# Kernel tuning notes

Hardware: AMD Instinct MI355X
Metric: run time of the kernel (lower is better)

Reference implementation:

```python
import jax, jax.numpy as jnp
import numpy as np

N = 8192  # number of nodes
F = 8     # feature dim


def setup_inputs() -> dict:
    key = jax.random.key(0)
    ks = jax.random.split(key, 24)
    inp = {
        "adj": jax.random.uniform(ks[0], (N, N), jnp.float32),
        "dist_from_prev": jax.random.uniform(ks[1], (N,), jnp.float32),
        "dist_to_start": jax.random.uniform(ks[2], (N,), jnp.float32),
    }
    dims = {"l0": (2, F), "l1": (F, F), "pol": (F, 1), "val": (F, 1)}
    i = 3
    for name, (din, dout) in dims.items():
        inp[f"W1_{name}"] = jax.random.normal(ks[i], (din, dout), jnp.float32) * 0.3; i += 1
        inp[f"b1_{name}"] = jax.random.normal(ks[i], (dout,), jnp.float32) * 0.1; i += 1
        inp[f"W2_{name}"] = jax.random.normal(ks[i], (dout, dout), jnp.float32) * 0.3; i += 1
        inp[f"b2_{name}"] = jax.random.normal(ks[i], (dout,), jnp.float32) * 0.1; i += 1
    return inp


def _mlp(x, adj, W1, b1, W2, b2):
    # GIN-style layer: aggregate then 2-layer MLP
    h = adj @ x                     # [N, din] aggregation (memory bound)
    h = jax.nn.relu(h @ W1 + b1)    # [N, dout]
    return h @ W2 + b2              # [N, dout]


def reference(adj, dist_from_prev, dist_to_start,
              W1_l0, b1_l0, W2_l0, b2_l0,
              W1_l1, b1_l1, W2_l1, b2_l1,
              W1_pol, b1_pol, W2_pol, b2_pol,
              W1_val, b1_val, W2_val, b2_val):
    cur = jnp.stack([dist_from_prev, dist_to_start], axis=1)  # [N, 2]
    # hidden GIN layers + relu (dropout is identity in eval mode)
    cur = jax.nn.relu(_mlp(cur, adj, W1_l0, b1_l0, W2_l0, b2_l0))
    cur = jax.nn.relu(_mlp(cur, adj, W1_l1, b1_l1, W2_l1, b2_l1))
    policy = jax.nn.softmax(_mlp(cur, adj, W1_pol, b1_pol, W2_pol, b2_pol)[:, 0], axis=0)  # [N]
    value = _mlp(cur, adj, W1_val, b1_val, W2_val, b2_val)[:, 0]  # [N]
    m = value.mean()
    std = jnp.sqrt(jnp.mean((value - m) ** 2) + 1e-10)
    normalized_value = (value - m) / std
    return policy, normalized_value
```

## Files before the change

### kernel.cpp

```cpp
#include <hip/hip_runtime.h>
#include <hip/hip_bf16.h>
#include <math.h>

#define NN 8192
typedef unsigned int u32;
typedef unsigned char u8;

__device__ __forceinline__ u32 bf16_rtne(float f) {
  u32 u = __float_as_uint(f);
  return (u + 0x7fffu + ((u >> 16) & 1u)) >> 16;
}
__device__ __forceinline__ float bf_lo(u32 d) { return __uint_as_float(d << 16); }
__device__ __forceinline__ float bf_hi(u32 d) { return __uint_as_float(d & 0xffff0000u); }

__global__ __launch_bounds__(256) void pass1_kernel(
    const float* __restrict__ adj, u8* __restrict__ adj8,
    const float* __restrict__ dfp, const float* __restrict__ dts,
    const float* __restrict__ W1, const float* __restrict__ b1,
    const float* __restrict__ W2, const float* __restrict__ b2,
    float* __restrict__ cur) {
  const int wave = threadIdx.x >> 6, lane = threadIdx.x & 63;
  const int row0 = blockIdx.x * 16 + wave * 4;
  float acc0[4] = {0.f, 0.f, 0.f, 0.f};
  float acc1[4] = {0.f, 0.f, 0.f, 0.f};

  float4 A[4], Xp, Xs;
  {
    const int k = 4 * lane;
    Xp = *(const float4*)(dfp + k);
    Xs = *(const float4*)(dts + k);
#pragma unroll
    for (int r = 0; r < 4; ++r)
      A[r] = *(const float4*)(adj + (size_t)(row0 + r) * NN + k);
  }
  for (int k0 = 0; k0 < NN; k0 += 256) {
    float4 B[4], Yp, Ys;
    if (k0 + 256 < NN) {
      const int k = k0 + 256 + 4 * lane;
      Yp = *(const float4*)(dfp + k);
      Ys = *(const float4*)(dts + k);
#pragma unroll
      for (int r = 0; r < 4; ++r)
        B[r] = *(const float4*)(adj + (size_t)(row0 + r) * NN + k);
    } else {
      Yp = Xp; Ys = Xs;
#pragma unroll
      for (int r = 0; r < 4; ++r) B[r] = A[r];
    }
    const float pv[4] = {Xp.x, Xp.y, Xp.z, Xp.w};
    const float sv[4] = {Xs.x, Xs.y, Xs.z, Xs.w};
#pragma unroll
    for (int r = 0; r < 4; ++r) {
      const float av[4] = {A[r].x, A[r].y, A[r].z, A[r].w};
#pragma unroll
      for (int c = 0; c < 4; ++c) {
        acc0[r] = fmaf(av[c], pv[c], acc0[r]);
        acc1[r] = fmaf(av[c], sv[c], acc1[r]);
      }
      u32 q0 = (u32)fmaf(av[0], 255.f, 0.5f);
      u32 q1 = (u32)fmaf(av[1], 255.f, 0.5f);
      u32 q2 = (u32)fmaf(av[2], 255.f, 0.5f);
      u32 q3 = (u32)fmaf(av[3], 255.f, 0.5f);
      ((u32*)(adj8 + (size_t)(row0 + r) * NN + k0))[lane] =
          q0 | (q1 << 8) | (q2 << 16) | (q3 << 24);
    }
#pragma unroll
    for (int r = 0; r < 4; ++r) A[r] = B[r];
    Xp = Yp; Xs = Ys;
  }
#pragma unroll
  for (int r = 0; r < 4; ++r) {
    for (int off = 32; off; off >>= 1) {
      acc0[r] += __shfl_xor(acc0[r], off, 64);
      acc1[r] += __shfl_xor(acc1[r], off, 64);
    }
  }
  const int j = lane & 7;
#pragma unroll
  for (int r = 0; r < 4; ++r) {
    float z = fmaf(acc0[r], W1[0 * 8 + j], fmaf(acc1[r], W1[1 * 8 + j], b1[j]));
    z = fmaxf(z, 0.f);
    float o = b2[j];
#pragma unroll
    for (int jj = 0; jj < 8; ++jj)
      o = fmaf(__shfl(z, jj, 64), W2[jj * 8 + j], o);
    if (lane < 8) cur[(size_t)(row0 + r) * 8 + j] = fmaxf(o, 0.f);
  }
}

template <int HEADS>
__global__ __launch_bounds__(512) void pass23_kernel(
    const u8* __restrict__ adj8, const float* __restrict__ x,
    const float* __restrict__ W1, const float* __restrict__ b1,
    const float* __restrict__ W2, const float* __restrict__ b2,
    const float* __restrict__ W1v, const float* __restrict__ b1v,
    const float* __restrict__ W2v, const float* __restrict__ b2v,
    float* __restrict__ out0, float* __restrict__ out1) {
  __shared__ u32 xT[8][NN / 2];
  const int tid = threadIdx.x;
  const int wave = tid >> 6, lane = tid & 63;
  const int row0 = blockIdx.x * 32 + wave * 4;

  uint4 A[4];
#pragma unroll
  for (int r = 0; r < 4; ++r)
    A[r] = *(const uint4*)(adj8 + (size_t)(row0 + r) * NN + 16 * lane);

  const float inv255 = 1.f / 255.f;
  for (int p = tid; p < NN / 2; p += 512) {
    const float* r0 = x + (size_t)p * 16;
    float4 a0 = *(const float4*)(r0);
    float4 b0 = *(const float4*)(r0 + 4);
    float4 a1 = *(const float4*)(r0 + 8);
    float4 c1 = *(const float4*)(r0 + 12);
    const float e0[8] = {a0.x, a0.y, a0.z, a0.w, b0.x, b0.y, b0.z, b0.w};
    const float e1[8] = {a1.x, a1.y, a1.z, a1.w, c1.x, c1.y, c1.z, c1.w};
#pragma unroll
    for (int jj = 0; jj < 8; ++jj)
      xT[jj][p] = bf16_rtne(e0[jj] * inv255) | (bf16_rtne(e1[jj] * inv255) << 16);
  }
  __syncthreads();

  float acc[4][8] = {};
  for (int k0 = 0; k0 < NN; k0 += 1024) {
    uint4 B[4];
    if (k0 + 1024 < NN) {
#pragma unroll
      for (int r = 0; r < 4; ++r)
        B[r] = *(const uint4*)(adj8 + (size_t)(row0 + r) * NN + (k0 + 1024) +
                               16 * lane);
    } else {
#pragma unroll
      for (int r = 0; r < 4; ++r) B[r] = A[r];
    }
    float av[4][16];
#pragma unroll
    for (int r = 0; r < 4; ++r) {
      const u32 dw[4] = {A[r].x, A[r].y, A[r].z, A[r].w};
#pragma unroll
      for (int t = 0; t < 16; ++t)
        av[r][t] = (float)((dw[t >> 2] >> (8 * (t & 3))) & 0xffu);
    }
    const u32* xrow;
#pragma unroll
    for (int jj = 0; jj < 8; ++jj) {
      xrow = &xT[jj][0];
      uint4 xp0 = *((const uint4*)xrow + (k0 >> 3) + 2 * lane);
      uint4 xp1 = *((const uint4*)xrow + (k0 >> 3) + 2 * lane + 1);
      float xf[16];
      xf[0] = bf_lo(xp0.x);  xf[1] = bf_hi(xp0.x);
      xf[2] = bf_lo(xp0.y);  xf[3] = bf_hi(xp0.y);
      xf[4] = bf_lo(xp0.z);  xf[5] = bf_hi(xp0.z);
      xf[6] = bf_lo(xp0.w);  xf[7] = bf_hi(xp0.w);
      xf[8] = bf_lo(xp1.x);  xf[9] = bf_hi(xp1.x);
      xf[10] = bf_lo(xp1.y); xf[11] = bf_hi(xp1.y);
      xf[12] = bf_lo(xp1.z); xf[13] = bf_hi(xp1.z);
      xf[14] = bf_lo(xp1.w); xf[15] = bf_hi(xp1.w);
#pragma unroll
      for (int r = 0; r < 4; ++r)
#pragma unroll
        for (int t = 0; t < 16; ++t)
          acc[r][jj] = fmaf(av[r][t], xf[t], acc[r][jj]);
    }
#pragma unroll
    for (int r = 0; r < 4; ++r) A[r] = B[r];
  }
#pragma unroll
  for (int r = 0; r < 4; ++r)
#pragma unroll
    for (int jj = 0; jj < 8; ++jj)
      for (int off = 32; off; off >>= 1)
        acc[r][jj] += __shfl_xor(acc[r][jj], off, 64);

  if (HEADS == 0) {
    const int j = lane & 7;
#pragma unroll
    for (int r = 0; r < 4; ++r) {
      float z = b1[j];
#pragma unroll
      for (int d = 0; d < 8; ++d) z = fmaf(acc[r][d], W1[d * 8 + j], z);
      z = fmaxf(z, 0.f);
      float o = b2[j];
#pragma unroll
      for (int jj = 0; jj < 8; ++jj)
        o = fmaf(__shfl(z, jj, 64), W2[jj * 8 + j], o);
      if (lane < 8) out0[(size_t)(row0 + r) * 8 + j] = fmaxf(o, 0.f);
    }
  } else {
    if (lane == 0) {
#pragma unroll
      for (int r = 0; r < 4; ++r) {
        float zp = b1[0], zv = b1v[0];
#pragma unroll
        for (int d = 0; d < 8; ++d) {
          zp = fmaf(acc[r][d], W1[d], zp);
          zv = fmaf(acc[r][d], W1v[d], zv);
        }
        zp = fmaxf(zp, 0.f);
        zv = fmaxf(zv, 0.f);
        out0[row0 + r] = fmaf(zp, W2[0], b2[0]);
        out1[row0 + r] = fmaf(zv, W2v[0], b2v[0]);
      }
    }
  }
}

__global__ __launch_bounds__(1024) void reduce_finalize_kernel(
    float* __restrict__ out) {
  const int tid = threadIdx.x, wave = tid >> 6, lane = tid & 63;
  __shared__ float sa[16], sb[16], sc[4];

  float4 l0 = *(const float4*)(out + tid * 8);
  float4 l1 = *(const float4*)(out + tid * 8 + 4);
  float4 v0 = *(const float4*)(out + NN + tid * 8);
  float4 v1 = *(const float4*)(out + NN + tid * 8 + 4);
  const float lv[8] = {l0.x, l0.y, l0.z, l0.w, l1.x, l1.y, l1.z, l1.w};
  const float vv[8] = {v0.x, v0.y, v0.z, v0.w, v1.x, v1.y, v1.z, v1.w};

  float m = -3.4e38f, s = 0.f;
#pragma unroll
  for (int i = 0; i < 8; ++i) {
    m = fmaxf(m, lv[i]);
    s += vv[i];
  }
  for (int off = 32; off; off >>= 1) {
    m = fmaxf(m, __shfl_xor(m, off, 64));
    s += __shfl_xor(s, off, 64);
  }
  if (lane == 0) { sa[wave] = m; sb[wave] = s; }
  __syncthreads();
  if (tid == 0) {
    float mm = sa[0], ss = sb[0];
    for (int i = 1; i < 16; ++i) { mm = fmaxf(mm, sa[i]); ss += sb[i]; }
    sc[0] = mm; sc[1] = ss * (1.f / NN);
  }
  __syncthreads();
  m = sc[0];
  const float mean = sc[1];

  float el[8];
  float e = 0.f, v2 = 0.f;
#pragma unroll
  for (int i = 0; i < 8; ++i) {
    el[i] = expf(lv[i] - m);
    e += el[i];
    float d = vv[i] - mean;
    v2 = fmaf(d, d, v2);
  }
  for (int off = 32; off; off >>= 1) {
    e += __shfl_xor(e, off, 64);
    v2 += __shfl_xor(v2, off, 64);
  }
  if (lane == 0) { sa[wave] = e; sb[wave] = v2; }
  __syncthreads();
  if (tid == 0) {
    float ee = sa[0], vvv = sb[0];
    for (int i = 1; i < 16; ++i) { ee += sa[i]; vvv += sb[i]; }
    sc[2] = 1.f / ee;
    sc[3] = 1.f / sqrtf(vvv * (1.f / NN) + 1e-10f);
  }
  __syncthreads();
  const float inv_e = sc[2], inv_std = sc[3];
  float4 o0, o1, w0, w1;
  o0.x = el[0] * inv_e; o0.y = el[1] * inv_e;
  o0.z = el[2] * inv_e; o0.w = el[3] * inv_e;
  o1.x = el[4] * inv_e; o1.y = el[5] * inv_e;
  o1.z = el[6] * inv_e; o1.w = el[7] * inv_e;
  w0.x = (vv[0] - mean) * inv_std; w0.y = (vv[1] - mean) * inv_std;
  w0.z = (vv[2] - mean) * inv_std; w0.w = (vv[3] - mean) * inv_std;
  w1.x = (vv[4] - mean) * inv_std; w1.y = (vv[5] - mean) * inv_std;
  w1.z = (vv[6] - mean) * inv_std; w1.w = (vv[7] - mean) * inv_std;
  *(float4*)(out + tid * 8) = o0;
  *(float4*)(out + tid * 8 + 4) = o1;
  *(float4*)(out + NN + tid * 8) = w0;
  *(float4*)(out + NN + tid * 8 + 4) = w1;
}

extern "C" void kernel_launch(void* const* d_in, const int* in_sizes, int n_in,
                              void* d_out, int out_size, void* d_ws,
                              size_t ws_size, hipStream_t stream) {
  const float* adj = (const float*)d_in[0];
  const float* dfp = (const float*)d_in[1];
  const float* dts = (const float*)d_in[2];
  const float* W1_l0 = (const float*)d_in[3];
  const float* b1_l0 = (const float*)d_in[4];
  const float* W2_l0 = (const float*)d_in[5];
  const float* b2_l0 = (const float*)d_in[6];
  const float* W1_l1 = (const float*)d_in[7];
  const float* b1_l1 = (const float*)d_in[8];
  const float* W2_l1 = (const float*)d_in[9];
  const float* b2_l1 = (const float*)d_in[10];
  const float* W1_pol = (const float*)d_in[11];
  const float* b1_pol = (const float*)d_in[12];
  const float* W2_pol = (const float*)d_in[13];
  const float* b2_pol = (const float*)d_in[14];
  const float* W1_val = (const float*)d_in[15];
  const float* b1_val = (const float*)d_in[16];
  const float* W2_val = (const float*)d_in[17];
  const float* b2_val = (const float*)d_in[18];

  u8* adj8 = (u8*)d_ws;
  float* curA = (float*)((char*)d_ws + (size_t)NN * NN);
  float* curB = curA + NN * 8;
  float* logits = (float*)d_out;
  float* value = logits + NN;

  pass1_kernel<<<NN / 16, 256, 0, stream>>>(adj, adj8, dfp, dts, W1_l0, b1_l0,
                                            W2_l0, b2_l0, curA);
  pass23_kernel<0><<<NN / 32, 512, 0, stream>>>(
      adj8, curA, W1_l1, b1_l1, W2_l1, b2_l1, W1_l1, b1_l1, W2_l1, b2_l1,
      curB, curB);
  pass23_kernel<1><<<NN / 32, 512, 0, stream>>>(
      adj8, curB, W1_pol, b1_pol, W2_pol, b2_pol, W1_val, b1_val, W2_val,
      b2_val, logits, value);
  reduce_finalize_kernel<<<1, 1024, 0, stream>>>((float*)d_out);
}
```

Baseline: 152.4 us.

## Quantize features to uint8 per-column and use integer dot4 for aggregation

The bf16 feature staging and the float FMAs on dequantized adjacency bytes are replaced by per-column uint8 quantization of the features. The scale comes from a global max gathered through per-block partial maxima written by the previous kernel. The aggregation then runs as packed 8-bit integer dot products (udot4) with u32 accumulators, which greatly cuts ALU work per adjacency byte, and is rescaled to float at the end. In exchange, the features lose precision (8 bits instead of bf16), and there is extra work for a transpose in shared memory and for the cross-block max reduction.

```diff
diff --git a/kernel.cpp b/kernel.cpp
--- a/kernel.cpp
+++ b/kernel.cpp
@@ -1,26 +1,31 @@
 #include <hip/hip_runtime.h>
-#include <hip/hip_bf16.h>
 #include <math.h>
 
 #define NN 8192
 typedef unsigned int u32;
 typedef unsigned char u8;
 
-__device__ __forceinline__ u32 bf16_rtne(float f) {
-  u32 u = __float_as_uint(f);
-  return (u + 0x7fffu + ((u >> 16) & 1u)) >> 16;
-}
-__device__ __forceinline__ float bf_lo(u32 d) { return __uint_as_float(d << 16); }
-__device__ __forceinline__ float bf_hi(u32 d) { return __uint_as_float(d & 0xffff0000u); }
+__device__ __forceinline__ u32 dot4(u32 a, u32 b, u32 c) {
+#if __has_builtin(__builtin_amdgcn_udot4)
+  return __builtin_amdgcn_udot4(a, b, c, false);
+#else
+  c += (a & 0xffu) * (b & 0xffu);
+  c += ((a >> 8) & 0xffu) * ((b >> 8) & 0xffu);
+  c += ((a >> 16) & 0xffu) * ((b >> 16) & 0xffu);
+  c += (a >> 24) * (b >> 24);
+  return c;
+#endif
+}
 
 __global__ __launch_bounds__(256) void pass1_kernel(
     const float* __restrict__ adj, u8* __restrict__ adj8,
     const float* __restrict__ dfp, const float* __restrict__ dts,
     const float* __restrict__ W1, const float* __restrict__ b1,
     const float* __restrict__ W2, const float* __restrict__ b2,
-    float* __restrict__ cur) {
+    float* __restrict__ cur, float* __restrict__ partial) {
   const int wave = threadIdx.x >> 6, lane = threadIdx.x & 63;
   const int row0 = blockIdx.x * 16 + wave * 4;
+  __shared__ float w1red[4][8];
   float acc0[4] = {0.f, 0.f, 0.f, 0.f};
   float acc1[4] = {0.f, 0.f, 0.f, 0.f};
 
@@ -76,6 +81,7 @@
     }
   }
   const int j = lane & 7;
+  float mx = 0.f;
 #pragma unroll
   for (int r = 0; r < 4; ++r) {
     float z = fmaf(acc0[r], W1[0 * 8 + j], fmaf(acc1[r], W1[1 * 8 + j], b1[j]));
@@ -84,19 +90,33 @@
 #pragma unroll
     for (int jj = 0; jj < 8; ++jj)
       o = fmaf(__shfl(z, jj, 64), W2[jj * 8 + j], o);
-    if (lane < 8) cur[(size_t)(row0 + r) * 8 + j] = fmaxf(o, 0.f);
+    float val = fmaxf(o, 0.f);
+    if (lane < 8) cur[(size_t)(row0 + r) * 8 + j] = val;
+    mx = fmaxf(mx, val);
+  }
+  if (lane < 8) w1red[wave][lane] = mx;
+  __syncthreads();
+  if (wave == 0 && lane < 8) {
+    float m2 = fmaxf(fmaxf(w1red[0][lane], w1red[1][lane]),
+                     fmaxf(w1red[2][lane], w1red[3][lane]));
+    partial[blockIdx.x * 8 + lane] = m2;
   }
 }
 
 template <int HEADS>
 __global__ __launch_bounds__(512) void pass23_kernel(
     const u8* __restrict__ adj8, const float* __restrict__ x,
+    const float* __restrict__ partial, int nprod,
     const float* __restrict__ W1, const float* __restrict__ b1,
     const float* __restrict__ W2, const float* __restrict__ b2,
     const float* __restrict__ W1v, const float* __restrict__ b1v,
     const float* __restrict__ W2v, const float* __restrict__ b2v,
-    float* __restrict__ out0, float* __restrict__ out1) {
-  __shared__ u32 xT[8][NN / 2];
+    float* __restrict__ out0, float* __restrict__ out1,
+    float* __restrict__ partial_out) {
+  __shared__ u32 sxR[NN * 2];
+  __shared__ u32 sxT[8 * 2048];
+  __shared__ float swred[8][8];
+  __shared__ float sqs[8], sds[8];
   const int tid = threadIdx.x;
   const int wave = tid >> 6, lane = tid & 63;
   const int row0 = blockIdx.x * 32 + wave * 4;
@@ -106,22 +126,64 @@
   for (int r = 0; r < 4; ++r)
     A[r] = *(const uint4*)(adj8 + (size_t)(row0 + r) * NN + 16 * lane);
 
-  const float inv255 = 1.f / 255.f;
-  for (int p = tid; p < NN / 2; p += 512) {
-    const float* r0 = x + (size_t)p * 16;
-    float4 a0 = *(const float4*)(r0);
-    float4 b0 = *(const float4*)(r0 + 4);
-    float4 a1 = *(const float4*)(r0 + 8);
-    float4 c1 = *(const float4*)(r0 + 12);
-    const float e0[8] = {a0.x, a0.y, a0.z, a0.w, b0.x, b0.y, b0.z, b0.w};
-    const float e1[8] = {a1.x, a1.y, a1.z, a1.w, c1.x, c1.y, c1.z, c1.w};
-#pragma unroll
-    for (int jj = 0; jj < 8; ++jj)
-      xT[jj][p] = bf16_rtne(e0[jj] * inv255) | (bf16_rtne(e1[jj] * inv255) << 16);
-  }
-  __syncthreads();
-
-  float acc[4][8] = {};
+  float pm[8] = {0.f, 0.f, 0.f, 0.f, 0.f, 0.f, 0.f, 0.f};
+  if (tid < nprod) {
+    float4 a = *(const float4*)(partial + tid * 8);
+    float4 b = *(const float4*)(partial + tid * 8 + 4);
+    pm[0] = a.x; pm[1] = a.y; pm[2] = a.z; pm[3] = a.w;
+    pm[4] = b.x; pm[5] = b.y; pm[6] = b.z; pm[7] = b.w;
+  }
+  for (int off = 32; off; off >>= 1)
+#pragma unroll
+    for (int j = 0; j < 8; ++j) pm[j] = fmaxf(pm[j], __shfl_xor(pm[j], off, 64));
+  if (lane == 0)
+#pragma unroll
+    for (int j = 0; j < 8; ++j) swred[wave][j] = pm[j];
+  __syncthreads();
+  if (tid < 8) {
+    float m2 = 0.f;
+#pragma unroll
+    for (int w = 0; w < 8; ++w) m2 = fmaxf(m2, swred[w][tid]);
+    m2 = fmaxf(m2, 1e-20f);
+    sqs[tid] = 255.f / m2;
+    sds[tid] = m2 / 65025.f;
+  }
+  __syncthreads();
+
+  float qs[8];
+#pragma unroll
+  for (int j = 0; j < 8; ++j) qs[j] = sqs[j];
+  for (int base = 0; base < NN; base += 512) {
+    const int row = base + tid;
+    float4 a = *(const float4*)(x + (size_t)row * 8);
+    float4 b = *(const float4*)(x + (size_t)row * 8 + 4);
+    u32 q0 = (u32)fmaf(a.x, qs[0], 0.5f), q1 = (u32)fmaf(a.y, qs[1], 0.5f);
+    u32 q2 = (u32)fmaf(a.z, qs[2], 0.5f), q3 = (u32)fmaf(a.w, qs[3], 0.5f);
+    u32 q4 = (u32)fmaf(b.x, qs[4], 0.5f), q5 = (u32)fmaf(b.y, qs[5], 0.5f);
+    u32 q6 = (u32)fmaf(b.z, qs[6], 0.5f), q7 = (u32)fmaf(b.w, qs[7], 0.5f);
+    uint2 pk;
+    pk.x = q0 | (q1 << 8) | (q2 << 16) | (q3 << 24);
+    pk.y = q4 | (q5 << 8) | (q6 << 16) | (q7 << 24);
+    ((uint2*)sxR)[row] = pk;
+  }
+  __syncthreads();
+
+  {
+    const int jj = tid & 7, g = tid >> 3;
+    const int dw = jj >> 2, sh = 8 * (jj & 3);
+#pragma unroll
+    for (int i = 0; i < 32; ++i) {
+      const int p = g + 64 * i;
+      u32 w = 0;
+#pragma unroll
+      for (int m = 0; m < 4; ++m)
+        w |= (((sxR[(4 * p + m) * 2 + dw] >> sh) & 0xffu) << (8 * m));
+      sxT[jj * 2048 + p] = w;
+    }
+  }
+  __syncthreads();
+
+  u32 acc[4][8] = {};
   for (int k0 = 0; k0 < NN; k0 += 1024) {
     uint4 B[4];
     if (k0 + 1024 < NN) {
@@ -133,34 +195,21 @@
 #pragma unroll
       for (int r = 0; r < 4; ++r) B[r] = A[r];
     }
-    float av[4][16];
+    uint4 xq[8];
+#pragma unroll
+    for (int jj = 0; jj < 8; ++jj)
+      xq[jj] = ((const uint4*)sxT)[jj * 512 + (k0 >> 4) + lane];
 #pragma unroll
     for (int r = 0; r < 4; ++r) {
-      const u32 dw[4] = {A[r].x, A[r].y, A[r].z, A[r].w};
-#pragma unroll
-      for (int t = 0; t < 16; ++t)
-        av[r][t] = (float)((dw[t >> 2] >> (8 * (t & 3))) & 0xffu);
-    }
-    const u32* xrow;
-#pragma unroll
-    for (int jj = 0; jj < 8; ++jj) {
-      xrow = &xT[jj][0];
-      uint4 xp0 = *((const uint4*)xrow + (k0 >> 3) + 2 * lane);
-      uint4 xp1 = *((const uint4*)xrow + (k0 >> 3) + 2 * lane + 1);
-      float xf[16];
-      xf[0] = bf_lo(xp0.x);  xf[1] = bf_hi(xp0.x);
-      xf[2] = bf_lo(xp0.y);  xf[3] = bf_hi(xp0.y);
-      xf[4] = bf_lo(xp0.z);  xf[5] = bf_hi(xp0.z);
-      xf[6] = bf_lo(xp0.w);  xf[7] = bf_hi(xp0.w);
-      xf[8] = bf_lo(xp1.x);  xf[9] = bf_hi(xp1.x);
-      xf[10] = bf_lo(xp1.y); xf[11] = bf_hi(xp1.y);
-      xf[12] = bf_lo(xp1.z); xf[13] = bf_hi(xp1.z);
-      xf[14] = bf_lo(xp1.w); xf[15] = bf_hi(xp1.w);
-#pragma unroll
-      for (int r = 0; r < 4; ++r)
-#pragma unroll
-        for (int t = 0; t < 16; ++t)
-          acc[r][jj] = fmaf(av[r][t], xf[t], acc[r][jj]);
+#pragma unroll
+      for (int jj = 0; jj < 8; ++jj) {
+        u32 c = acc[r][jj];
+        c = dot4(A[r].x, xq[jj].x, c);
+        c = dot4(A[r].y, xq[jj].y, c);
+        c = dot4(A[r].z, xq[jj].z, c);
+        c = dot4(A[r].w, xq[jj].w, c);
+        acc[r][jj] = c;
+      }
     }
 #pragma unroll
     for (int r = 0; r < 4; ++r) A[r] = B[r];
@@ -170,21 +219,40 @@
 #pragma unroll
     for (int jj = 0; jj < 8; ++jj)
       for (int off = 32; off; off >>= 1)
-        acc[r][jj] += __shfl_xor(acc[r][jj], off, 64);
+        acc[r][jj] += (u32)__shfl_xor((int)acc[r][jj], off, 64);
+  float dsc[8];
+#pragma unroll
+  for (int j = 0; j < 8; ++j) dsc[j] = sds[j];
+  float h[4][8];
+#pragma unroll
+  for (int r = 0; r < 4; ++r)
+#pragma unroll
+    for (int jj = 0; jj < 8; ++jj) h[r][jj] = (float)acc[r][jj] * dsc[jj];
 
   if (HEADS == 0) {
     const int j = lane & 7;
+    float mxv = 0.f;
 #pragma unroll
     for (int r = 0; r < 4; ++r) {
       float z = b1[j];
 #pragma unroll
-      for (int d = 0; d < 8; ++d) z = fmaf(acc[r][d], W1[d * 8 + j], z);
+      for (int d = 0; d < 8; ++d) z = fmaf(h[r][d], W1[d * 8 + j], z);
       z = fmaxf(z, 0.f);
       float o = b2[j];
 #pragma unroll
       for (int jj = 0; jj < 8; ++jj)
         o = fmaf(__shfl(z, jj, 64), W2[jj * 8 + j], o);
-      if (lane < 8) out0[(size_t)(row0 + r) * 8 + j] = fmaxf(o, 0.f);
+      float val = fmaxf(o, 0.f);
+      if (lane < 8) out0[(size_t)(row0 + r) * 8 + j] = val;
+      mxv = fmaxf(mxv, val);
+    }
+    if (lane < 8) swred[wave][lane] = mxv;
+    __syncthreads();
+    if (wave == 0 && lane < 8) {
+      float m2 = 0.f;
+#pragma unroll
+      for (int w = 0; w < 8; ++w) m2 = fmaxf(m2, swred[w][lane]);
+      partial_out[blockIdx.x * 8 + lane] = m2;
     }
   } else {
     if (lane == 0) {
@@ -193,8 +261,8 @@
         float zp = b1[0], zv = b1v[0];
 #pragma unroll
         for (int d = 0; d < 8; ++d) {
-          zp = fmaf(acc[r][d], W1[d], zp);
-          zv = fmaf(acc[r][d], W1v[d], zv);
+          zp = fmaf(h[r][d], W1[d], zp);
+          zv = fmaf(h[r][d], W1v[d], zv);
         }
         zp = fmaxf(zp, 0.f);
         zv = fmaxf(zv, 0.f);
@@ -302,16 +370,18 @@
   u8* adj8 = (u8*)d_ws;
   float* curA = (float*)((char*)d_ws + (size_t)NN * NN);
   float* curB = curA + NN * 8;
+  float* partialA = curB + NN * 8;
+  float* partialB = partialA + 512 * 8;
   float* logits = (float*)d_out;
   float* value = logits + NN;
 
   pass1_kernel<<<NN / 16, 256, 0, stream>>>(adj, adj8, dfp, dts, W1_l0, b1_l0,
-                                            W2_l0, b2_l0, curA);
+                                            W2_l0, b2_l0, curA, partialA);
   pass23_kernel<0><<<NN / 32, 512, 0, stream>>>(
-      adj8, curA, W1_l1, b1_l1, W2_l1, b2_l1, W1_l1, b1_l1, W2_l1, b2_l1,
-      curB, curB);
+      adj8, curA, partialA, 512, W1_l1, b1_l1, W2_l1, b2_l1, W1_l1, b1_l1,
+      W2_l1, b2_l1, curB, curB, partialB);
   pass23_kernel<1><<<NN / 32, 512, 0, stream>>>(
-      adj8, curB, W1_pol, b1_pol, W2_pol, b2_pol, W1_val, b1_val, W2_val,
-      b2_val, logits, value);
+      adj8, curB, partialB, 256, W1_pol, b1_pol, W2_pol, b2_pol, W1_val,
+      b1_val, W2_val, b2_val, logits, value, partialB);
   reduce_finalize_kernel<<<1, 1024, 0, stream>>>((float*)d_out);
 }
```

Measured after the change: 145.9 us. -4.3%, faster.
